# Performance work log

Hardware: AMD Instinct MI355X
Metric: run time of the kernel (lower is better)

## Reference

```python
import jax, jax.numpy as jnp
import numpy as np

GROUPS = 2
EPS = 1e-5


def channel_shuffle(x, groups=2):
    b, c, h, w = x.shape
    x = x.reshape(b, groups, c // groups, h, w)
    x = jnp.transpose(x, (0, 2, 1, 3, 4))
    return x.reshape(b, c, h, w)


def binarize_weight(w):
    # w: (O, I/g, k, k). scaling_factor = mean |w| over (in,kh,kw), detached.
    scale = jax.lax.stop_gradient(jnp.mean(jnp.abs(w), axis=(1, 2, 3), keepdims=True))
    bw = scale * jnp.sign(w)
    cl = jnp.clip(w, -1.0, 1.0)
    # STE: forward value = bw, gradient flows through clamp
    return jax.lax.stop_gradient(bw) - jax.lax.stop_gradient(cl) + cl


@jax.custom_vjp
def bin_act(x):
    return jnp.sign(x)


def _bin_act_fwd(x):
    return jnp.sign(x), x


def _bin_act_bwd(x, g):
    scale = jnp.where((x >= 1.0) | (x <= -1.0), 0.01, 1.0)
    return (g * scale,)


bin_act.defvjp(_bin_act_fwd, _bin_act_bwd)


def grouped_bin_conv(x, w, pad):
    return jax.lax.conv_general_dilated(
        x, binarize_weight(w), window_strides=(1, 1),
        padding=[(pad, pad), (pad, pad)],
        dimension_numbers=('NCHW', 'OIHW', 'NCHW'),
        feature_group_count=GROUPS)


def batchnorm(x, gamma, beta):
    # training-mode BN: biased batch statistics over (N,H,W)
    mu = jnp.mean(x, axis=(0, 2, 3), keepdims=True)
    var = jnp.mean((x - mu) ** 2, axis=(0, 2, 3), keepdims=True)
    xn = (x - mu) * jax.lax.rsqrt(var + EPS)
    return xn * gamma[None, :, None, None] + beta[None, :, None, None]


def add_bias(x, b):
    return x + b[None, :, None, None]


def prelu(x, a):
    return jnp.where(x >= 0, x, a[None, :, None, None] * x)


def setup_inputs() -> dict:
    key = jax.random.key(0)
    ks = jax.random.split(key, 4)
    C, half = 256, 128
    x = jax.random.normal(ks[0], (32, C, 56, 56), dtype=jnp.float32)
    # two BinaryConvs (64,128,3,3) stacked -> grouped (128,128,3,3)
    w3 = jax.random.uniform(ks[1], (half, C // GROUPS, 3, 3), dtype=jnp.float32) * 0.001
    w1 = jax.random.uniform(ks[2], (half, C // GROUPS, 1, 1), dtype=jnp.float32) * 0.001
    z = jnp.zeros((C,), jnp.float32)
    return {
        'x': x, 'w3': w3, 'w1': w1,
        'b1': z, 'g1': jnp.ones((half,), jnp.float32), 'be1': jnp.zeros((half,), jnp.float32),
        'b2_1': z, 'a2': jnp.full((C,), 0.25, jnp.float32), 'b2_2': z,
        'b3_1': z, 'g3': jnp.ones((half,), jnp.float32), 'be3': jnp.zeros((half,), jnp.float32),
        'b4_1': z, 'a4': jnp.full((C,), 0.25, jnp.float32), 'b4_2': z,
    }


def reference(x, w3, w1, b1, g1, be1, b2_1, a2, b2_2, b3_1, g3, be3, b4_1, a4, b4_2):
    half = w3.shape[0]  # out_channel // 2 = 128
    x = channel_shuffle(x, GROUPS)
    x1 = bin_act(add_bias(x, b1))
    x1 = batchnorm(grouped_bin_conv(x1, w3, pad=1), g1, be1)
    x1_res = x[:, half:]
    x1 = x1 + x[:, :half]
    x2 = jnp.concatenate([x1, x1_res], axis=1)
    x2 = add_bias(prelu(add_bias(x2, b2_1), a2), b2_2)
    x2 = add_bias(x2, b3_1)
    x3 = bin_act(x2)
    x3 = batchnorm(grouped_bin_conv(x3, w1, pad=0), g3, be3)
    x3_res = x2[:, half:]
    x3 = x3 + x2[:, :half]
    x4 = jnp.concatenate([x3, x3_res], axis=1)
    x5 = add_bias(prelu(add_bias(x4, b4_1), a4), b4_2)
    return x5
```

## Files before the change

kernel.cpp:

```cpp
#include <hip/hip_runtime.h>
#include <stdint.h>

typedef unsigned short ushort_t;
typedef unsigned int uint_t;
typedef _Float16 half_t;

typedef float  float4_t __attribute__((ext_vector_type(4)));
typedef _Float16 half4_t __attribute__((ext_vector_type(4)));

#define B_N 32
#define C_N 256
#define HALF_N 128
#define H_N 56
#define W_N 56
#define HW_N 3136
#define NPIX (B_N * HW_N)
#define EPS_D 1e-5
#define W3S 40
#define PWS 16

__global__ void prep_kernel(const float* __restrict__ w3, const float* __restrict__ w1,
                            uint_t* __restrict__ wbits3, uint_t* __restrict__ wbits1,
                            uint_t* __restrict__ popcw3,
                            double* __restrict__ scale3, double* __restrict__ scale1,
                            double* __restrict__ sums1, double* __restrict__ sums2,
                            uint_t* __restrict__ oflags) {
    __shared__ double red[128];
    __shared__ int ipw[2][9];
    __shared__ int flsh[2];
    int t = threadIdx.x;
    int blk = blockIdx.x;
    int lane = t & 63;
    int wv = t >> 6;
    if (blk == 0) {
        sums1[t] = 0.0; sums1[128 + t] = 0.0;
        sums2[t] = 0.0; sums2[128 + t] = 0.0;
    }
    if (blk < 128) {
        int o = blk;
        double acc = 0.0;
        int anynp = 0;
        #pragma unroll
        for (int j = 0; j < 9; ++j) {
            float v = w3[o * 1152 + t * 9 + j];
            acc += fabs((double)v);
            anynp |= (v <= 0.f) ? 1 : 0;
            unsigned long long b = __ballot(v > 0.f);
            if (lane == 0) {
                wbits3[o * W3S + j * 4 + wv * 2 + 0] = (uint_t)b;
                wbits3[o * W3S + j * 4 + wv * 2 + 1] = (uint_t)(b >> 32);
                ipw[wv][j] = __popcll(b);
            }
        }
        unsigned long long m = __ballot(anynp != 0);
        if (lane == 0) flsh[wv] = (m != 0ull) ? 1 : 0;
        red[t] = acc; __syncthreads();
        for (int s = 64; s > 0; s >>= 1) { if (t < s) red[t] += red[t + s]; __syncthreads(); }
        if (t == 0) { scale3[o] = red[0] / 1152.0; oflags[o] = (uint_t)(flsh[0] | flsh[1]); }
        if (t < 9) popcw3[o * PWS + t] = (uint_t)(ipw[0][t] + ipw[1][t]);
    } else {
        int o = blk - 128;
        float v = w1[o * 128 + t];
        unsigned long long b = __ballot(v > 0.f);
        unsigned long long m = __ballot(v <= 0.f);
        if (lane == 0) {
            wbits1[o * 8 + wv * 2 + 0] = (uint_t)b;
            wbits1[o * 8 + wv * 2 + 1] = (uint_t)(b >> 32);
            flsh[wv] = (m != 0ull) ? 1 : 0;
        }
        red[t] = fabs((double)v); __syncthreads();
        for (int s = 64; s > 0; s >>= 1) { if (t < s) red[t] += red[t + s]; __syncthreads(); }
        if (t == 0) { scale1[o] = red[0] / 128.0; oflags[128 + o] = (uint_t)(flsh[0] | flsh[1]); }
    }
}

__global__ __launch_bounds__(256) void sign1_kernel(const float* __restrict__ x,
                                                    const float* __restrict__ b1,
                                                    uint_t* __restrict__ vb,
                                                    const uint_t* __restrict__ oflags,
                                                    uint_t* __restrict__ fin) {
    __shared__ int fl[4];
    int t = threadIdx.x;
    if (blockIdx.x == 0 && blockIdx.y == 0) {
        int lane = t & 63, wv4 = t >> 6;
        uint_t f = oflags[t];
        unsigned long long m = __ballot(f != 0u);
        if (lane == 0) fl[wv4] = (m != 0ull) ? 1 : 0;
        __syncthreads();
        if (t == 0) { fin[0] = (uint_t)(fl[0] | fl[1]); fin[1] = (uint_t)(fl[2] | fl[3]); }
    }
    int p = blockIdx.x * 256 + t;
    int cb = blockIdx.y * 64;
    int b = p / HW_N;
    int hw = p - b * HW_N;
    const float* xb = x + (size_t)b * C_N * HW_N + hw;
    #pragma unroll
    for (int wq = 0; wq < 2; ++wq) {
        uint_t bits = 0u;
        #pragma unroll
        for (int j = 0; j < 32; ++j) {
            int c = cb + wq * 32 + j;
            int src = ((c & 1) << 7) + (c >> 1);
            double v = (double)xb[(size_t)src * HW_N] + (double)b1[c];
            bits |= (v > 0.0) ? (1u << j) : 0u;
        }
        vb[(size_t)((cb >> 5) + wq) * NPIX + p] = bits;
    }
}

__global__ __launch_bounds__(256) void conv3_kernel(const uint_t* __restrict__ vb,
                                                    const uint_t* __restrict__ wbits3,
                                                    const uint_t* __restrict__ popcw3,
                                                    half_t* __restrict__ yh,
                                                    double* __restrict__ sums,
                                                    const uint_t* __restrict__ fin) {
    __shared__ short dlds[32][258];
    __shared__ int partS[8][32];
    __shared__ int partS2[8][32];
    int t = threadIdx.x;
    int lane = t & 63;
    int wv = t >> 6;
    bool fast = (fin[0] == 0u);
    int yb = blockIdx.y;
    if (fast && (yb & 1)) return;
    int g = yb >> 1;
    int oh = yb & 1;
    int o0 = g * 64 + oh * 32;
    int p = blockIdx.x * 256 + t;
    int hw = p % HW_N;
    int h = hw / W_N;
    int w = hw - h * W_N;
    const uint_t* vbase = vb + (size_t)g * 4 * NPIX;

    uint_t v[9][4];
    int inv[9];
    int nvalid = 0;
    #pragma unroll
    for (int j = 0; j < 9; ++j) {
        int kh = j / 3 - 1, kw = j - (j / 3) * 3 - 1;
        int hh = h + kh, ww = w + kw;
        bool valid = (hh >= 0) && (hh < H_N) && (ww >= 0) && (ww < W_N);
        inv[j] = valid ? 0 : 1;
        nvalid += valid ? 1 : 0;
        int off = p + kh * W_N + kw;
        #pragma unroll
        for (int q = 0; q < 4; ++q)
            v[j][q] = valid ? vbase[(size_t)q * NPIX + off] : 0u;
    }
    int base = 128 * nvalid;

    if (fast) {
        int P = 0;
        #pragma unroll
        for (int j = 0; j < 9; ++j)
            #pragma unroll
            for (int q = 0; q < 4; ++q)
                P += __popc(v[j][q]);
        int dot = 2 * P - base;
        yh[(size_t)o0 * NPIX + p] = (half_t)(float)dot;
        int s = dot, s2 = dot * dot;
        #pragma unroll
        for (int off = 32; off > 0; off >>= 1) {
            s  += __shfl_xor(s, off);
            s2 += __shfl_xor(s2, off);
        }
        if (lane == 0) { partS[0][wv] = s; partS2[0][wv] = s2; }
        __syncthreads();
        if (t == 0) {
            partS[1][0]  = partS[0][0] + partS[0][1] + partS[0][2] + partS[0][3];
            partS2[1][0] = partS2[0][0] + partS2[0][1] + partS2[0][2] + partS2[0][3];
        }
        __syncthreads();
        if (t < 64) {
            atomicAdd(&sums[o0 + t], (double)partS[1][0]);
            atomicAdd(&sums[128 + o0 + t], (double)partS2[1][0]);
        }
        return;
    }

    half_t* yrow = yh + (size_t)o0 * NPIX + p;
    for (int oi = 0; oi < 32; ++oi) {
        const uint_t* wo = wbits3 + (size_t)(o0 + oi) * W3S;
        const uint_t* pw = popcw3 + (size_t)(o0 + oi) * PWS;
        int acc = 0;
        #pragma unroll
        for (int j = 0; j < 9; ++j)
            #pragma unroll
            for (int q = 0; q < 4; ++q)
                acc += __popc(v[j][q] ^ wo[j * 4 + q]);
        int corr = 0;
        #pragma unroll
        for (int j = 0; j < 9; ++j) corr += inv[j] * (int)pw[j];
        int dot = base - 2 * (acc - corr);
        yrow[(size_t)oi * NPIX] = (half_t)(float)dot;
        dlds[oi][t] = (short)dot;
    }
    __syncthreads();
    {
        int o = t & 31, seg = t >> 5;
        const int* r32 = (const int*)(&dlds[o][seg * 32]);
        int S = 0, S2 = 0;
        #pragma unroll
        for (int j = 0; j < 16; ++j) {
            int pr = r32[j];
            int d0 = (int)(short)(pr & 0xffff);
            int d1 = pr >> 16;
            S += d0 + d1; S2 += d0 * d0 + d1 * d1;
        }
        partS[seg][o] = S; partS2[seg][o] = S2;
    }
    __syncthreads();
    if (t < 32) {
        int S = 0, S2 = 0;
        #pragma unroll
        for (int s8 = 0; s8 < 8; ++s8) { S += partS[s8][t]; S2 += partS2[s8][t]; }
        int c = o0 + t;
        atomicAdd(&sums[c], (double)S);
        atomicAdd(&sums[128 + c], (double)S2);
    }
}

__device__ __forceinline__ void coef_entry(const double* __restrict__ sums,
                                           const double* __restrict__ scale,
                                           const float* __restrict__ gamma,
                                           const float* __restrict__ beta,
                                           int c, double* coefL) {
    double M = (double)NPIX;
    double mean = sums[c] / M;
    double var = sums[128 + c] / M - mean * mean;
    double s = scale[c];
    double r = 1.0 / sqrt(s * s * var + EPS_D);
    double g = (double)gamma[c];
    coefL[c] = s * r * g;
    coefL[128 + c] = (double)beta[c] - s * mean * r * g;
}

__device__ __forceinline__ void coef_entry_f(const double* __restrict__ sums,
                                             const double* __restrict__ scale,
                                             const float* __restrict__ gamma,
                                             const float* __restrict__ beta,
                                             int c, float* cf) {
    double M = (double)NPIX;
    double mean = sums[c] / M;
    double var = sums[128 + c] / M - mean * mean;
    double s = scale[c];
    double r = 1.0 / sqrt(s * s * var + EPS_D);
    double g = (double)gamma[c];
    cf[c] = (float)(s * r * g);
    cf[128 + c] = (float)((double)beta[c] - s * mean * r * g);
}

__device__ __forceinline__ double x2_val(double xs, double K, bool hasy,
                                         const double* coef1, int c,
                                         const float* __restrict__ b2_1, const float* __restrict__ a2,
                                         const float* __restrict__ b2_2, const float* __restrict__ b3_1) {
    int ci = c & 127;
    double t = hasy ? (coef1[ci] * K + coef1[128 + ci] + xs) : xs;
    t += (double)b2_1[c];
    double a = (double)a2[c];
    t = (t >= 0.0) ? t : a * t;
    t += (double)b2_2[c];
    t += (double)b3_1[c];
    return t;
}

__global__ __launch_bounds__(256) void x2c1_kernel(
        const float* __restrict__ x, const half_t* __restrict__ y1h,
        const double* __restrict__ sums1, const double* __restrict__ scale3,
        const float* __restrict__ g1, const float* __restrict__ be1,
        const float* __restrict__ b2_1, const float* __restrict__ a2,
        const float* __restrict__ b2_2, const float* __restrict__ b3_1,
        const uint_t* __restrict__ wbits1,
        half_t* __restrict__ y3h, double* __restrict__ sums2,
        const uint_t* __restrict__ fin) {
    __shared__ double coefL[256];
    __shared__ short dst[32][258];
    __shared__ int partS[8][32];
    __shared__ int partS2[8][32];
    int t = threadIdx.x;
    int lane = t & 63;
    int wv = t >> 6;
    int g = blockIdx.y;
    bool fast3 = (fin[0] == 0u);
    bool fast1 = (fin[1] == 0u);
    if (g == 0 && t < 128) coef_entry(sums1, scale3, g1, be1, t, coefL);
    __syncthreads();

    int p = blockIdx.x * 256 + t;
    int b = p / HW_N;
    int hw = p - b * HW_N;
    const float* xb = x + (size_t)b * C_N * HW_N + hw;
    int c0 = g * 128;

    uint_t w0_, w1_, w2_, w3_;
    if (g == 0) {
        if (fast3) {
            double K0  = (double)(float)y1h[p];
            double K64 = (double)(float)y1h[(size_t)64 * NPIX + p];
            #pragma unroll
            for (int wq = 0; wq < 4; ++wq) {
                uint_t bits = 0u;
                double Kc = (wq < 2) ? K0 : K64;
                #pragma unroll
                for (int j = 0; j < 32; ++j) {
                    int c = wq * 32 + j;
                    int src = ((c & 1) << 7) + (c >> 1);
                    double xs = (double)xb[(size_t)src * HW_N];
                    double v = x2_val(xs, Kc, true, coefL, c, b2_1, a2, b2_2, b3_1);
                    bits |= (v > 0.0) ? (1u << j) : 0u;
                }
                if (wq == 0) w0_ = bits; else if (wq == 1) w1_ = bits;
                else if (wq == 2) w2_ = bits; else w3_ = bits;
            }
        } else {
            #pragma unroll
            for (int wq = 0; wq < 4; ++wq) {
                uint_t bits = 0u;
                #pragma unroll
                for (int j = 0; j < 32; ++j) {
                    int c = wq * 32 + j;
                    int src = ((c & 1) << 7) + (c >> 1);
                    double xs = (double)xb[(size_t)src * HW_N];
                    double K = (double)(float)y1h[(size_t)c * NPIX + p];
                    double v = x2_val(xs, K, true, coefL, c, b2_1, a2, b2_2, b3_1);
                    bits |= (v > 0.0) ? (1u << j) : 0u;
                }
                if (wq == 0) w0_ = bits; else if (wq == 1) w1_ = bits;
                else if (wq == 2) w2_ = bits; else w3_ = bits;
            }
        }
    } else {
        #pragma unroll
        for (int wq = 0; wq < 4; ++wq) {
            uint_t bits = 0u;
            #pragma unroll
            for (int j = 0; j < 32; ++j) {
                int c = c0 + wq * 32 + j;
                int src = ((c & 1) << 7) + (c >> 1);
                double xs = (double)xb[(size_t)src * HW_N];
                double v = x2_val(xs, 0.0, false, coefL, c, b2_1, a2, b2_2, b3_1);
                bits |= (v > 0.0) ? (1u << j) : 0u;
            }
            if (wq == 0) w0_ = bits; else if (wq == 1) w1_ = bits;
            else if (wq == 2) w2_ = bits; else w3_ = bits;
        }
    }

    int obase = g * 64;
    if (fast1) {
        int P = __popc(w0_) + __popc(w1_) + __popc(w2_) + __popc(w3_);
        int dotv = 2 * P - 128;
        y3h[(size_t)obase * NPIX + p] = (half_t)(float)dotv;
        int s = dotv, s2 = dotv * dotv;
        #pragma unroll
        for (int off = 32; off > 0; off >>= 1) {
            s  += __shfl_xor(s, off);
            s2 += __shfl_xor(s2, off);
        }
        if (lane == 0) { partS[0][wv] = s; partS2[0][wv] = s2; }
        __syncthreads();
        if (t == 0) {
            partS[1][0]  = partS[0][0] + partS[0][1] + partS[0][2] + partS[0][3];
            partS2[1][0] = partS2[0][0] + partS2[0][1] + partS2[0][2] + partS2[0][3];
        }
        __syncthreads();
        if (t < 64) {
            atomicAdd(&sums2[obase + t], (double)partS[1][0]);
            atomicAdd(&sums2[128 + obase + t], (double)partS2[1][0]);
        }
        return;
    }

    #pragma unroll
    for (int ch = 0; ch < 2; ++ch) {
        #pragma unroll
        for (int oi = 0; oi < 32; ++oi) {
            int o = obase + ch * 32 + oi;
            const uint_t* wo = wbits1 + (size_t)o * 8;
            int acc = __popc(w0_ ^ wo[0]) + __popc(w1_ ^ wo[1])
                    + __popc(w2_ ^ wo[2]) + __popc(w3_ ^ wo[3]);
            int dot = 128 - 2 * acc;
            y3h[(size_t)o * NPIX + p] = (half_t)(float)dot;
            dst[oi][t] = (short)dot;
        }
        __syncthreads();
        {
            int o = t & 31, seg = t >> 5;
            const int* r32 = (const int*)(&dst[o][seg * 32]);
            int S = 0, S2 = 0;
            #pragma unroll
            for (int j = 0; j < 16; ++j) {
                int pr = r32[j];
                int d0 = (int)(short)(pr & 0xffff);
                int d1 = pr >> 16;
                S += d0 + d1; S2 += d0 * d0 + d1 * d1;
            }
            partS[seg][o] = S; partS2[seg][o] = S2;
        }
        __syncthreads();
        if (t < 32) {
            int S = 0, S2 = 0;
            #pragma unroll
            for (int s8 = 0; s8 < 8; ++s8) { S += partS[s8][t]; S2 += partS2[s8][t]; }
            int c = obase + ch * 32 + t;
            atomicAdd(&sums2[c], (double)S);
            atomicAdd(&sums2[128 + c], (double)S2);
        }
        __syncthreads();
    }
}

__global__ __launch_bounds__(256) void out_kernel(
        const float* __restrict__ x, const half_t* __restrict__ y1h,
        const half_t* __restrict__ y3h,
        const double* __restrict__ sums1, const double* __restrict__ scale3,
        const float* __restrict__ g1, const float* __restrict__ be1,
        const double* __restrict__ sums2, const double* __restrict__ scale1,
        const float* __restrict__ g3, const float* __restrict__ be3,
        const float* __restrict__ b2_1, const float* __restrict__ a2,
        const float* __restrict__ b2_2, const float* __restrict__ b3_1,
        const float* __restrict__ b4_1, const float* __restrict__ a4,
        const float* __restrict__ b4_2, float* __restrict__ out,
        const uint_t* __restrict__ fin) {
    __shared__ float c1f[256];
    __shared__ float c3f[256];
    int t = threadIdx.x;
    if (t < 128) coef_entry_f(sums1, scale3, g1, be1, t, c1f);
    else coef_entry_f(sums2, scale1, g3, be3, t - 128, c3f);
    __syncthreads();
    int c = blockIdx.y;
    bool h1 = (c < 128);
    int src = ((c & 1) << 7) + (c >> 1);
    int ci = c & 127;
    int y1slice = (fin[0] == 0u) ? ((ci < 64) ? 0 : 64) : ci;
    int y3slice = (fin[1] == 0u) ? ((ci < 64) ? 0 : 64) : ci;
    float b21 = b2_1[c], aa2v = a2[c], b23 = b2_2[c] + b3_1[c];
    float b41 = b4_1[c], aa4v = a4[c], b42 = b4_2[c];
    float c1 = c1f[ci], c1b = c1f[128 + ci];
    float c3 = c3f[ci], c3b = c3f[128 + ci];
    const half_t* y1p = y1h + (size_t)y1slice * NPIX;
    const half_t* y3p = y3h + (size_t)y3slice * NPIX;
    #pragma unroll
    for (int i = 0; i < 2; ++i) {
        int p = blockIdx.x * 2048 + i * 1024 + t * 4;
        int b = p / HW_N;
        int hw = p - b * HW_N;
        float4_t xs = *(const float4_t*)(x + ((size_t)b * C_N + src) * HW_N + hw);
        half4_t y1v = *(const half4_t*)(y1p + p);
        half4_t y3v = *(const half4_t*)(y3p + p);
        float4_t ov;
        #pragma unroll
        for (int k = 0; k < 4; ++k) {
            float v = h1 ? fmaf(c1, (float)y1v[k], c1b) + xs[k] : xs[k];
            v += b21;
            v = (v >= 0.f) ? v : aa2v * v;
            v += b23;
            float t2 = v;
            if (h1) v = fmaf(c3, (float)y3v[k], c3b) + t2;
            v += b41;
            v = (v >= 0.f) ? v : aa4v * v;
            v += b42;
            ov[k] = v;
        }
        *(float4_t*)(out + ((size_t)b * C_N + c) * HW_N + hw) = ov;
    }
}

extern "C" void kernel_launch(void* const* d_in, const int* in_sizes, int n_in,
                              void* d_out, int out_size, void* d_ws, size_t ws_size,
                              hipStream_t stream) {
    const float* x    = (const float*)d_in[0];
    const float* w3   = (const float*)d_in[1];
    const float* w1   = (const float*)d_in[2];
    const float* b1   = (const float*)d_in[3];
    const float* g1   = (const float*)d_in[4];
    const float* be1  = (const float*)d_in[5];
    const float* b2_1 = (const float*)d_in[6];
    const float* a2   = (const float*)d_in[7];
    const float* b2_2 = (const float*)d_in[8];
    const float* b3_1 = (const float*)d_in[9];
    const float* g3   = (const float*)d_in[10];
    const float* be3  = (const float*)d_in[11];
    const float* b4_1 = (const float*)d_in[12];
    const float* a4   = (const float*)d_in[13];
    const float* b4_2 = (const float*)d_in[14];

    char* ws = (char*)d_ws;
    half_t* y1h    = (half_t*)(ws + 0);
    half_t* y3h    = (half_t*)(ws + 25690112);
    uint_t* wbits3 = (uint_t*)(ws + 51380224);
    uint_t* wbits1 = (uint_t*)(ws + 51400704);
    uint_t* popcw3 = (uint_t*)(ws + 51404800);
    double* scale3 = (double*)(ws + 51412992);
    double* scale1 = (double*)(ws + 51414016);
    double* sums1  = (double*)(ws + 51415040);
    double* sums2  = (double*)(ws + 51417088);
    uint_t* oflags = (uint_t*)(ws + 51419136);
    uint_t* fin    = (uint_t*)(ws + 51420160);

    uint_t* vb1 = (uint_t*)((char*)d_out + 0);
    float*  outp = (float*)d_out;

    prep_kernel<<<256, 128, 0, stream>>>(w3, w1, wbits3, wbits1, popcw3,
                                         scale3, scale1, sums1, sums2, oflags);
    sign1_kernel<<<dim3(NPIX / 256, 4), 256, 0, stream>>>(x, b1, vb1, oflags, fin);
    conv3_kernel<<<dim3(NPIX / 256, 4), 256, 0, stream>>>(vb1, wbits3, popcw3, y1h, sums1, fin);
    x2c1_kernel<<<dim3(NPIX / 256, 2), 256, 0, stream>>>(x, y1h, sums1, scale3, g1, be1,
                                                         b2_1, a2, b2_2, b3_1,
                                                         wbits1, y3h, sums2, fin);
    out_kernel<<<dim3(NPIX / 2048, 256), 256, 0, stream>>>(x, y1h, y3h,
                                                           sums1, scale3, g1, be1,
                                                           sums2, scale1, g3, be3,
                                                           b2_1, a2, b2_2, b3_1,
                                                           b4_1, a4, b4_2, outp, fin);
}
```

Measured before the change: 272.9 us.

## Fuse passthrough-half output into x2c1 and vectorize sign1 over pixel pairs

The x2c1 kernel now writes the final output for the upper 128 channels (which need no second conv) directly while it computes their sign bits, so out_kernel only launches over the lower 128 channels and skips re-reading x for the passthrough half. The sign1 kernel now handles two adjacent pixels per thread with float2 loads and a uint2 store, and uses 32 channels per block instead of 64. This cuts global traffic and launch work, but the fused output stores in x2c1 are scalar and strided per channel, which may coalesce worse than out_kernel's float4 stores. Writing out from x2c1 is safe because vb1 aliases only the first bytes of d_out, which conv3 has already consumed, and x2c1's writes land in the upper channels.

```diff
diff --git a/kernel.cpp b/kernel.cpp
--- a/kernel.cpp
+++ b/kernel.cpp
@@ -6,7 +6,9 @@
 typedef _Float16 half_t;
 
 typedef float  float4_t __attribute__((ext_vector_type(4)));
+typedef float  float2_t __attribute__((ext_vector_type(2)));
 typedef _Float16 half4_t __attribute__((ext_vector_type(4)));
+typedef uint_t uint2_t  __attribute__((ext_vector_type(2)));
 
 #define B_N 32
 #define C_N 256
@@ -89,23 +91,23 @@
         __syncthreads();
         if (t == 0) { fin[0] = (uint_t)(fl[0] | fl[1]); fin[1] = (uint_t)(fl[2] | fl[3]); }
     }
-    int p = blockIdx.x * 256 + t;
-    int cb = blockIdx.y * 64;
+    int p = blockIdx.x * 512 + t * 2;
+    int cb = blockIdx.y * 32;
     int b = p / HW_N;
     int hw = p - b * HW_N;
     const float* xb = x + (size_t)b * C_N * HW_N + hw;
+    uint_t w0 = 0, w1 = 0;
     #pragma unroll
-    for (int wq = 0; wq < 2; ++wq) {
-        uint_t bits = 0u;
-        #pragma unroll
-        for (int j = 0; j < 32; ++j) {
-            int c = cb + wq * 32 + j;
-            int src = ((c & 1) << 7) + (c >> 1);
-            double v = (double)xb[(size_t)src * HW_N] + (double)b1[c];
-            bits |= (v > 0.0) ? (1u << j) : 0u;
-        }
-        vb[(size_t)((cb >> 5) + wq) * NPIX + p] = bits;
-    }
+    for (int j = 0; j < 32; ++j) {
+        int c = cb + j;
+        int src = ((c & 1) << 7) + (c >> 1);
+        float2_t xv = *(const float2_t*)(xb + (size_t)src * HW_N);
+        double bc = (double)b1[c];
+        if ((double)xv[0] + bc > 0.0) w0 |= (1u << j);
+        if ((double)xv[1] + bc > 0.0) w1 |= (1u << j);
+    }
+    uint2_t o2; o2[0] = w0; o2[1] = w1;
+    *(uint2_t*)(vb + (size_t)(cb >> 5) * NPIX + p) = o2;
 }
 
 __global__ __launch_bounds__(256) void conv3_kernel(const uint_t* __restrict__ vb,
@@ -272,6 +274,8 @@
         const float* __restrict__ b2_2, const float* __restrict__ b3_1,
         const uint_t* __restrict__ wbits1,
         half_t* __restrict__ y3h, double* __restrict__ sums2,
+        const float* __restrict__ b4_1, const float* __restrict__ a4,
+        const float* __restrict__ b4_2, float* __restrict__ out,
         const uint_t* __restrict__ fin) {
     __shared__ double coefL[256];
     __shared__ short dst[32][258];
@@ -340,6 +344,10 @@
                 double xs = (double)xb[(size_t)src * HW_N];
                 double v = x2_val(xs, 0.0, false, coefL, c, b2_1, a2, b2_2, b3_1);
                 bits |= (v > 0.0) ? (1u << j) : 0u;
+                float f0 = (float)v + b4_1[c];
+                f0 = (f0 >= 0.f) ? f0 : a4[c] * f0;
+                f0 += b4_2[c];
+                out[((size_t)b * C_N + c) * HW_N + hw] = f0;
             }
             if (wq == 0) w0_ = bits; else if (wq == 1) w1_ = bits;
             else if (wq == 2) w2_ = bits; else w3_ = bits;
@@ -429,15 +437,13 @@
     else coef_entry_f(sums2, scale1, g3, be3, t - 128, c3f);
     __syncthreads();
     int c = blockIdx.y;
-    bool h1 = (c < 128);
     int src = ((c & 1) << 7) + (c >> 1);
-    int ci = c & 127;
-    int y1slice = (fin[0] == 0u) ? ((ci < 64) ? 0 : 64) : ci;
-    int y3slice = (fin[1] == 0u) ? ((ci < 64) ? 0 : 64) : ci;
+    int y1slice = (fin[0] == 0u) ? ((c < 64) ? 0 : 64) : c;
+    int y3slice = (fin[1] == 0u) ? ((c < 64) ? 0 : 64) : c;
     float b21 = b2_1[c], aa2v = a2[c], b23 = b2_2[c] + b3_1[c];
     float b41 = b4_1[c], aa4v = a4[c], b42 = b4_2[c];
-    float c1 = c1f[ci], c1b = c1f[128 + ci];
-    float c3 = c3f[ci], c3b = c3f[128 + ci];
+    float c1 = c1f[c], c1b = c1f[128 + c];
+    float c3 = c3f[c], c3b = c3f[128 + c];
     const half_t* y1p = y1h + (size_t)y1slice * NPIX;
     const half_t* y3p = y3h + (size_t)y3slice * NPIX;
     #pragma unroll
@@ -451,12 +457,12 @@
         float4_t ov;
         #pragma unroll
         for (int k = 0; k < 4; ++k) {
-            float v = h1 ? fmaf(c1, (float)y1v[k], c1b) + xs[k] : xs[k];
+            float v = fmaf(c1, (float)y1v[k], c1b) + xs[k];
             v += b21;
             v = (v >= 0.f) ? v : aa2v * v;
             v += b23;
             float t2 = v;
-            if (h1) v = fmaf(c3, (float)y3v[k], c3b) + t2;
+            v = fmaf(c3, (float)y3v[k], c3b) + t2;
             v += b41;
             v = (v >= 0.f) ? v : aa4v * v;
             v += b42;
@@ -503,12 +509,13 @@
 
     prep_kernel<<<256, 128, 0, stream>>>(w3, w1, wbits3, wbits1, popcw3,
                                          scale3, scale1, sums1, sums2, oflags);
-    sign1_kernel<<<dim3(NPIX / 256, 4), 256, 0, stream>>>(x, b1, vb1, oflags, fin);
+    sign1_kernel<<<dim3(NPIX / 512, 8), 256, 0, stream>>>(x, b1, vb1, oflags, fin);
     conv3_kernel<<<dim3(NPIX / 256, 4), 256, 0, stream>>>(vb1, wbits3, popcw3, y1h, sums1, fin);
     x2c1_kernel<<<dim3(NPIX / 256, 2), 256, 0, stream>>>(x, y1h, sums1, scale3, g1, be1,
                                                          b2_1, a2, b2_2, b3_1,
-                                                         wbits1, y3h, sums2, fin);
-    out_kernel<<<dim3(NPIX / 2048, 256), 256, 0, stream>>>(x, y1h, y3h,
+                                                         wbits1, y3h, sums2,
+                                                         b4_1, a4, b4_2, outp, fin);
+    out_kernel<<<dim3(NPIX / 2048, 128), 256, 0, stream>>>(x, y1h, y3h,
                                                            sums1, scale3, g1, be1,
                                                            sums2, scale1, g3, be3,
                                                            b2_1, a2, b2_2, b3_1,
```

Result: slower. 345.3 us (+26.5%).
